# Performance work log

Hardware: AMD Instinct MI355X
Metric: run time of the kernel (lower is better)

The kernel has to match this reference:

```python
import jax, jax.numpy as jnp
import numpy as np

SEQ_LENGTH = 513
E = 512      # input_dim / embedding size
H = 1024     # hidden_dim
C = 512      # num_classes
B = 128      # batch


def setup_inputs() -> dict:
    key = jax.random.key(0)
    ks = jax.random.split(key, 12)

    def kaiming(k, shape):
        # kaiming_normal_ default: fan_in = shape[0] (fan computed on dim 1 of [out,in]; here params are [in,out] and torch uses fan_in=size(1)... torch fan_in for 2D = shape[1])
        fan_in = shape[1]
        std = np.sqrt(2.0 / fan_in)
        return jax.random.normal(k, shape, dtype=jnp.float32) * std

    inp = {
        "x": jax.random.randint(ks[0], (B, SEQ_LENGTH), 0, SEQ_LENGTH),
        "emb": jax.random.normal(ks[1], (SEQ_LENGTH, E), dtype=jnp.float32),
        "W_gx": kaiming(ks[2], (E, H)),
        "W_gh": kaiming(ks[3], (H, H)),
        "b_g": jnp.zeros((1, H), jnp.float32),
        "W_ix": kaiming(ks[4], (E, H)),
        "W_ih": kaiming(ks[5], (H, H)),
        "b_i": jnp.zeros((1, H), jnp.float32),
        "W_fx": kaiming(ks[6], (E, H)),
        "W_fh": kaiming(ks[7], (H, H)),
        "b_f": jnp.zeros((1, H), jnp.float32),
        "W_ox": kaiming(ks[8], (E, H)),
        "W_oh": kaiming(ks[9], (H, H)),
        "b_o": jnp.zeros((1, H), jnp.float32),
        "W_ph": kaiming(ks[10], (H, C)),
        "b_p": jnp.zeros((1, C), jnp.float32),
        "h_init": jnp.zeros((1, H), jnp.float32),
        "c_init": jnp.zeros((1, H), jnp.float32),
    }
    return inp


def reference(x, emb, W_gx, W_gh, b_g, W_ix, W_ih, b_i, W_fx, W_fh, b_f,
              W_ox, W_oh, b_o, W_ph, b_p, h_init, c_init):
    T = SEQ_LENGTH - 1  # module loops seq_length-1 steps
    embed_x = emb[x]                       # [B, SEQ_LENGTH, E]
    xs = jnp.swapaxes(embed_x[:, :T, :], 0, 1)  # [T, B, E]
    b = x.shape[0]
    h0 = jnp.broadcast_to(h_init, (b, H))
    c0 = jnp.broadcast_to(c_init, (b, H))

    def step(carry, e_t):
        h, c = carry
        g = jnp.tanh(e_t @ W_gx + h @ W_gh + b_g)
        i = jax.nn.sigmoid(e_t @ W_ix + h @ W_ih + b_i)
        f = jax.nn.sigmoid(e_t @ W_fx + h @ W_fh + b_f)
        o = jax.nn.sigmoid(e_t @ W_ox + h @ W_oh + b_o)
        c_new = g * i + c * f
        h_new = jnp.tanh(c_new) * o
        return (h_new, c_new), None

    (h_T, _), _ = jax.lax.scan(step, (h0, c0), xs)
    p_t = h_T @ W_ph + b_p                 # [B, C]
    return jax.nn.log_softmax(p_t, axis=1)
```

## Files before the change

### kernel.cpp

```cpp
#include <hip/hip_runtime.h>
#include <hip/hip_cooperative_groups.h>
#include <cmath>

namespace cg = cooperative_groups;

#define T_STEPS 512
#define NBLK 256

typedef _Float16 h8 __attribute__((ext_vector_type(8)));
typedef float f4 __attribute__((ext_vector_type(4)));
typedef int i32x4 __attribute__((ext_vector_type(4)));
typedef unsigned long long ull_t;

__device__ __forceinline__ float sigm(float v) { return 1.f / (1.f + __expf(-v)); }
__device__ __forceinline__ float tanh_fast(float v) { return 1.f - 2.f / (__expf(2.f * v) + 1.f); }

__global__ void pack_P(const float* __restrict__ emb,
                       const float* __restrict__ Wgx, const float* __restrict__ Wix,
                       const float* __restrict__ Wfx, const float* __restrict__ Wox,
                       const float* __restrict__ bg, const float* __restrict__ bi,
                       const float* __restrict__ bf_, const float* __restrict__ bo,
                       float* __restrict__ P) {
  __shared__ float es[8][512];
  const int vg = blockIdx.x;
  const int st = blockIdx.y;
  const int tid = threadIdx.x;
  for (int i = tid; i < 8 * 512; i += 256) {
    int vv = i >> 9, k = i & 511;
    int v = vg * 8 + vv;
    es[vv][k] = (v < 513) ? emb[v * 512 + k] : 0.f;
  }
  __syncthreads();
  const int c = st * 256 + tid;
  const int gate = c & 3, unit = c >> 2;
  const float* W = gate == 0 ? Wgx : gate == 1 ? Wix : gate == 2 ? Wfx : Wox;
  const float* bias = gate == 0 ? bg : gate == 1 ? bi : gate == 2 ? bf_ : bo;
  float acc[8];
  const float bv = bias[unit];
#pragma unroll
  for (int vv = 0; vv < 8; vv++) acc[vv] = bv;
  for (int k = 0; k < 512; k++) {
    float w = W[k * 1024 + unit];
#pragma unroll
    for (int vv = 0; vv < 8; vv++) acc[vv] += es[vv][k] * w;
  }
#pragma unroll
  for (int vv = 0; vv < 8; vv++) {
    int v = vg * 8 + vv;
    if (v < 513) P[(size_t)v * 4096 + c] = acc[vv];
  }
}

__global__ void pack_Wt(const float* __restrict__ Wgh, const float* __restrict__ Wih,
                        const float* __restrict__ Wfh, const float* __restrict__ Woh,
                        _Float16* __restrict__ Wt) {
  const int c = blockIdx.x;
  const int gate = c & 3, unit = c >> 2;
  const float* W = gate == 0 ? Wgh : gate == 1 ? Wih : gate == 2 ? Wfh : Woh;
  for (int k = threadIdx.x; k < 1024; k += 256)
    Wt[(size_t)c * 1024 + k] = (_Float16)W[k * 1024 + unit];
}

__launch_bounds__(512, 2)
__global__ void lstm_step_all(const int* __restrict__ x,
                              const float* __restrict__ P,
                              const _Float16* __restrict__ Wt,
                              _Float16* __restrict__ hbuf,
                              float* __restrict__ h32,
                              const float* __restrict__ h_init,
                              const float* __restrict__ c_init) {
  cg::grid_group grid = cg::this_grid();
  __shared__ _Float16 alds[16 * 1024];
  __shared__ float pre[16 * 132];
  const int tid = threadIdx.x;
  const int blk = blockIdx.x;
  const int grp = blk & 7;
  const int sub = blk >> 3;
  const int lane = tid & 63;
  const int wid = tid >> 6;
  const int l15 = lane & 15;
  const int gg = lane >> 4;
  const int kg = gg * 8;
  const int colbase = sub * 128;
  const int ubase = sub * 32;
  const int rowbase = grp * 16;
  const int arow = tid >> 5;
  const int agb = tid & 31;

  h8 bfr[32];
  {
    const _Float16* wp = Wt + (size_t)(colbase + wid * 16 + l15) * 1024 + kg;
#pragma unroll
    for (int s = 0; s < 32; s++) bfr[s] = *(const h8*)(wp + s * 32);
  }

  if (tid < 128) {
    int r16 = tid >> 3, q = tid & 7;
    union { _Float16 h[4]; ull_t u; } pk;
#pragma unroll
    for (int u = 0; u < 4; u++) pk.h[u] = (_Float16)h_init[ubase + q * 4 + u];
    pk.u &= 0xFFFEFFFEFFFEFFFEull;
    *(ull_t*)&hbuf[(size_t)(rowbase + r16) * 1024 + ubase + q * 4] = pk.u;
    *(ull_t*)&hbuf[(size_t)(128 * 1024) + (size_t)(rowbase + r16) * 1024 + ubase + q * 4] =
        0x0001000100010001ull;
  }
  const int grow = tid >> 5;
  const int gu = tid & 31;
  float cst = c_init[ubase + gu];
  const int abase = arow * 1024 + ((agb ^ (arow & 7)) * 8);
  grid.sync();

  for (int t = 0; t < T_STEPS; t++) {
    const _Float16* hc = hbuf + (t & 1) * (128 * 1024);
    _Float16* hn = hbuf + ((t + 1) & 1) * (128 * 1024);

    const int xv = x[(rowbase + grow) * 513 + t];
    const float* prow = P + (size_t)xv * 4096 + colbase + gu * 4;
    f4 pv = *(const f4*)(prow);

    const int tagm = (int)(0x00010001u * (unsigned)((t >> 1) & 1));
    i32x4 av0, av1, av2, av3;
    {
      const _Float16* pbase = &hc[(size_t)(rowbase + arow) * 1024 + agb * 8];
      for (;;) {
        asm volatile("global_load_dwordx4 %0, %1, off sc0 sc1"
                     : "=v"(av0) : "v"(pbase) : "memory");
        asm volatile("global_load_dwordx4 %0, %1, off offset:512 sc0 sc1"
                     : "=v"(av1) : "v"(pbase) : "memory");
        asm volatile("global_load_dwordx4 %0, %1, off offset:1024 sc0 sc1"
                     : "=v"(av2) : "v"(pbase) : "memory");
        asm volatile("global_load_dwordx4 %0, %1, off offset:1536 sc0 sc1"
                     : "=v"(av3) : "v"(pbase) : "memory");
        asm volatile("s_waitcnt vmcnt(0)" ::: "memory");
        bool ok = true;
#pragma unroll
        for (int j = 0; j < 4; j++) {
          ok &= ((av0[j] & 0x00010001) == tagm);
          ok &= ((av1[j] & 0x00010001) == tagm);
          ok &= ((av2[j] & 0x00010001) == tagm);
          ok &= ((av3[j] & 0x00010001) == tagm);
        }
        if (ok) break;
        __builtin_amdgcn_s_sleep(1);
      }
    }
    __builtin_amdgcn_sched_barrier(0);
    *(i32x4*)&alds[abase] = av0;
    *(i32x4*)&alds[abase + 256] = av1;
    *(i32x4*)&alds[abase + 512] = av2;
    *(i32x4*)&alds[abase + 768] = av3;
    __syncthreads();

    f4 ac0 = {0.f, 0.f, 0.f, 0.f}, ac1 = ac0, ac2 = ac0, ac3 = ac0;
#pragma unroll
    for (int s = 0; s < 32; s++) {
      int g = s * 4 + gg;
      h8 a = *(const h8*)&alds[l15 * 1024 + ((g ^ (l15 & 7)) * 8)];
      if ((s & 3) == 0) ac0 = __builtin_amdgcn_mfma_f32_16x16x32_f16(a, bfr[s], ac0, 0, 0, 0);
      else if ((s & 3) == 1) ac1 = __builtin_amdgcn_mfma_f32_16x16x32_f16(a, bfr[s], ac1, 0, 0, 0);
      else if ((s & 3) == 2) ac2 = __builtin_amdgcn_mfma_f32_16x16x32_f16(a, bfr[s], ac2, 0, 0, 0);
      else ac3 = __builtin_amdgcn_mfma_f32_16x16x32_f16(a, bfr[s], ac3, 0, 0, 0);
    }
    f4 acc = (ac0 + ac1) + (ac2 + ac3);
#pragma unroll
    for (int i = 0; i < 4; i++)
      pre[(gg * 4 + i) * 132 + wid * 16 + l15] = acc[i];
    __syncthreads();

    {
      f4 q = *(const f4*)&pre[grow * 132 + gu * 4];
      q += pv;
      float g_ = tanh_fast(q[0]);
      float i_ = sigm(q[1]);
      float f_ = sigm(q[2]);
      float o_ = sigm(q[3]);
      cst = g_ * i_ + cst * f_;
      float hv = tanh_fast(cst) * o_;
      if (t == T_STEPS - 1) {
        h32[(size_t)(rowbase + grow) * 1024 + ubase + gu] = hv;
      } else {
        const unsigned tagn = (unsigned)(((t + 1) >> 1) & 1);
        union { _Float16 hh; unsigned short us; } cv;
        cv.hh = (_Float16)hv;
        unsigned v0 = ((unsigned)cv.us & 0xFFFEu) | tagn;
        unsigned v1 = (unsigned)__shfl_down((int)v0, 1);
        unsigned lo = (v0 & 0xffffu) | (v1 << 16);
        unsigned lo2 = (unsigned)__shfl_down((int)lo, 2);
        if ((gu & 3) == 0) {
          ull_t pv8 = (ull_t)lo | ((ull_t)lo2 << 32);
          __hip_atomic_store((ull_t*)&hn[(size_t)(rowbase + grow) * 1024 + ubase + gu],
                             pv8, __ATOMIC_RELAXED, __HIP_MEMORY_SCOPE_AGENT);
        }
      }
    }
  }
}

__global__ void proj(const float* __restrict__ h32, const float* __restrict__ Wph,
                     const float* __restrict__ bp, float* __restrict__ logits) {
  const int b = blockIdx.x >> 1;
  const int cc = (blockIdx.x & 1) * 256 + threadIdx.x;
  const float* hrow = h32 + b * 1024;
  float acc = bp[cc];
#pragma unroll 4
  for (int k = 0; k < 1024; k++) acc += hrow[k] * Wph[k * 512 + cc];
  logits[b * 512 + cc] = acc;
}

__global__ void lsm(const float* __restrict__ logits, float* __restrict__ out) {
  const int b = blockIdx.x;
  const int tid = threadIdx.x;
  __shared__ float sm[4];
  __shared__ float se[4];
  float v0 = logits[b * 512 + tid];
  float v1 = logits[b * 512 + 256 + tid];
  float m = fmaxf(v0, v1);
  for (int o = 1; o < 64; o <<= 1) m = fmaxf(m, __shfl_xor(m, o, 64));
  if ((tid & 63) == 0) sm[tid >> 6] = m;
  __syncthreads();
  m = fmaxf(fmaxf(sm[0], sm[1]), fmaxf(sm[2], sm[3]));
  float e = expf(v0 - m) + expf(v1 - m);
  for (int o = 1; o < 64; o <<= 1) e += __shfl_xor(e, o, 64);
  if ((tid & 63) == 0) se[tid >> 6] = e;
  __syncthreads();
  float ls = logf(se[0] + se[1] + se[2] + se[3]) + m;
  out[b * 512 + tid] = v0 - ls;
  out[b * 512 + 256 + tid] = v1 - ls;
}

extern "C" void kernel_launch(void* const* d_in, const int* in_sizes, int n_in,
                              void* d_out, int out_size, void* d_ws, size_t ws_size,
                              hipStream_t stream) {
  const int* x = (const int*)d_in[0];
  const float* emb = (const float*)d_in[1];
  const float* Wgx = (const float*)d_in[2];
  const float* Wgh = (const float*)d_in[3];
  const float* bg = (const float*)d_in[4];
  const float* Wix = (const float*)d_in[5];
  const float* Wih = (const float*)d_in[6];
  const float* bi = (const float*)d_in[7];
  const float* Wfx = (const float*)d_in[8];
  const float* Wfh = (const float*)d_in[9];
  const float* bf = (const float*)d_in[10];
  const float* Wox = (const float*)d_in[11];
  const float* Woh = (const float*)d_in[12];
  const float* bo = (const float*)d_in[13];
  const float* Wph = (const float*)d_in[14];
  const float* bp = (const float*)d_in[15];
  const float* h_init = (const float*)d_in[16];
  const float* c_init = (const float*)d_in[17];

  char* ws = (char*)d_ws;
  float* P = (float*)ws;
  _Float16* Wt = (_Float16*)(ws + 8519680);
  _Float16* hbuf = (_Float16*)(ws + 8519680 + 8388608);
  float* h32 = (float*)(ws + 8519680 + 8388608 + 524288);
  float* logits = (float*)(ws + 8519680 + 8388608 + 524288 + 524288);

  pack_P<<<dim3(65, 16), 256, 0, stream>>>(emb, Wgx, Wix, Wfx, Wox, bg, bi, bf, bo, P);
  pack_Wt<<<4096, 256, 0, stream>>>(Wgh, Wih, Wfh, Woh, Wt);

  void* args[] = {(void*)&x, (void*)&P, (void*)&Wt, (void*)&hbuf,
                  (void*)&h32, (void*)&h_init, (void*)&c_init};
  hipLaunchCooperativeKernel((void*)lstm_step_all, dim3(NBLK), dim3(512), args, 0, stream);

  proj<<<256, 256, 0, stream>>>(h32, Wph, bp, logits);
  lsm<<<128, 256, 0, stream>>>(logits, (float*)d_out);
}
```

Baseline: 1.521 ms.

## Split recurrent matmul over K across waves with LDS partial-sum reduction

Each wave now takes a 128-wide slice of the hidden dimension and computes all 8 column tiles, instead of owning a 16-column tile across the full K. Operands are swapped so weights act as the A fragment, each wave reads only 4 h fragments from LDS instead of 32, and the 8 waves' partial sums go to a larger LDS buffer and are summed in the gate epilogue. The aim is to cut LDS read traffic and lengthen independent MFMA chains per wave. In exchange it needs 8x more LDS for partials and adds an 8-way reduction read per step.

```diff
diff --git a/kernel.cpp b/kernel.cpp
--- a/kernel.cpp
+++ b/kernel.cpp
@@ -71,7 +71,7 @@
                               const float* __restrict__ c_init) {
   cg::grid_group grid = cg::this_grid();
   __shared__ _Float16 alds[16 * 1024];
-  __shared__ float pre[16 * 132];
+  __shared__ float part[8 * 16 * 132];
   const int tid = threadIdx.x;
   const int blk = blockIdx.x;
   const int grp = blk & 7;
@@ -87,11 +87,14 @@
   const int arow = tid >> 5;
   const int agb = tid & 31;
 
-  h8 bfr[32];
+  h8 wfr[32];
   {
-    const _Float16* wp = Wt + (size_t)(colbase + wid * 16 + l15) * 1024 + kg;
-#pragma unroll
-    for (int s = 0; s < 32; s++) bfr[s] = *(const h8*)(wp + s * 32);
+    const _Float16* wp = Wt + (size_t)(colbase + l15) * 1024 + wid * 128 + kg;
+#pragma unroll
+    for (int ct = 0; ct < 8; ct++)
+#pragma unroll
+      for (int ks = 0; ks < 4; ks++)
+        wfr[ct * 4 + ks] = *(const h8*)(wp + (size_t)ct * 16 * 1024 + ks * 32);
   }
 
   if (tid < 128) {
@@ -151,25 +154,32 @@
     *(i32x4*)&alds[abase + 768] = av3;
     __syncthreads();
 
-    f4 ac0 = {0.f, 0.f, 0.f, 0.f}, ac1 = ac0, ac2 = ac0, ac3 = ac0;
-#pragma unroll
-    for (int s = 0; s < 32; s++) {
-      int g = s * 4 + gg;
-      h8 a = *(const h8*)&alds[l15 * 1024 + ((g ^ (l15 & 7)) * 8)];
-      if ((s & 3) == 0) ac0 = __builtin_amdgcn_mfma_f32_16x16x32_f16(a, bfr[s], ac0, 0, 0, 0);
-      else if ((s & 3) == 1) ac1 = __builtin_amdgcn_mfma_f32_16x16x32_f16(a, bfr[s], ac1, 0, 0, 0);
-      else if ((s & 3) == 2) ac2 = __builtin_amdgcn_mfma_f32_16x16x32_f16(a, bfr[s], ac2, 0, 0, 0);
-      else ac3 = __builtin_amdgcn_mfma_f32_16x16x32_f16(a, bfr[s], ac3, 0, 0, 0);
-    }
-    f4 acc = (ac0 + ac1) + (ac2 + ac3);
-#pragma unroll
-    for (int i = 0; i < 4; i++)
-      pre[(gg * 4 + i) * 132 + wid * 16 + l15] = acc[i];
+    h8 hfr[4];
+#pragma unroll
+    for (int ks = 0; ks < 4; ks++) {
+      int g = wid * 16 + ks * 4 + gg;
+      hfr[ks] = *(const h8*)&alds[l15 * 1024 + ((g ^ (l15 & 7)) * 8)];
+    }
+
+    f4 acc[8];
+#pragma unroll
+    for (int ct = 0; ct < 8; ct++) {
+      acc[ct] = (f4){0.f, 0.f, 0.f, 0.f};
+#pragma unroll
+      for (int ks = 0; ks < 4; ks++)
+        acc[ct] = __builtin_amdgcn_mfma_f32_16x16x32_f16(wfr[ct * 4 + ks], hfr[ks],
+                                                         acc[ct], 0, 0, 0);
+    }
+#pragma unroll
+    for (int ct = 0; ct < 8; ct++)
+      *(f4*)&part[(wid * 16 + l15) * 132 + ct * 16 + 4 * gg] = acc[ct];
     __syncthreads();
 
     {
-      f4 q = *(const f4*)&pre[grow * 132 + gu * 4];
-      q += pv;
+      f4 q = pv;
+#pragma unroll
+      for (int w = 0; w < 8; w++)
+        q += *(const f4*)&part[(w * 16 + grow) * 132 + gu * 4];
       float g_ = tanh_fast(q[0]);
       float i_ = sigm(q[1]);
       float f_ = sigm(q[2]);
```

Measured after the change: 1.387 ms. -8.8%, faster.
